# Kernel optimization log

Measured on AMD Instinct MI355X. Metric: run time of the kernel, lower is better.

Reference implementation:

```python
import jax, jax.numpy as jnp
from jax import lax
import numpy as np

INPUT_SCALE = 1.0
RES_SCALE = 1.0
RES_SIZE = 2048
INPUT_SIZE = 512
SEQ_LEN = 8192


def setup_inputs() -> dict:
    key = jax.random.key(0)
    k1, k2, k3, k4 = jax.random.split(key, 4)
    inp = jax.random.normal(k1, (SEQ_LEN, INPUT_SIZE), dtype=jnp.float32)
    state = jax.random.normal(k2, (RES_SIZE,), dtype=jnp.float32)
    W_in = jax.random.normal(k3, (RES_SIZE, INPUT_SIZE), dtype=jnp.float32)
    W_res = jax.random.normal(k4, (RES_SIZE, RES_SIZE), dtype=jnp.float32)
    return {"input": inp, "state": state, "W_in": W_in, "W_res": W_res}


def reference(input, state, W_in, W_res):
    # states[i+1] = tanh(input_scale * W_in @ input[i] + res_scale * W_res @ states[i]) / sqrt(res_size)
    inv_sqrt_n = jnp.asarray(1.0 / np.sqrt(RES_SIZE), dtype=input.dtype)
    # hoist all input projections into one GEMM: (seq_len, res_size)
    u = (INPUT_SCALE * input) @ W_in.T

    def step(s, u_t):
        s_new = jnp.tanh(u_t + RES_SCALE * (W_res @ s)) * inv_sqrt_n
        return s_new, s_new

    _, states = lax.scan(step, state, u)
    # prepend the initial state -> (seq_len+1, res_size)
    return jnp.concatenate([state[None, :], states], axis=0)
```

## Files before the change

### kernel.cpp

```cpp
#include <hip/hip_runtime.h>

#define T_SEQ   8192
#define N_RES   2048
#define K_IN    512

#define G_BLOCKS 64
#define B_THREADS 512
#define ROWS_PER_WAVE 4
#define ROWS_PER_BLOCK 32
static_assert(G_BLOCKS * ROWS_PER_BLOCK == N_RES, "row partition mismatch");

#define INV_SQRT_N 0.022097086912079612f

#define ENC_OFF 0.1f
#define ENC_THR 0.05f

typedef unsigned long long u64;
typedef unsigned int u32;
typedef float f32x2 __attribute__((ext_vector_type(2)));
typedef float f32x4 __attribute__((ext_vector_type(4)));

__device__ __forceinline__ float fast_tanh(float v) {
    float e = __expf(2.0f * v);
    return 1.0f - 2.0f / (e + 1.0f);
}

__device__ __forceinline__ void store_f4_coh(float* p, f32x4 v) {
    asm volatile("global_store_dwordx4 %0, %1, off sc0 sc1"
                 :: "v"(p), "v"(v) : "memory");
}
__device__ __forceinline__ f32x4 load_f4_coh(const float* p) {
    f32x4 r;
    asm volatile("global_load_dwordx4 %0, %1, off sc0 sc1\n\t"
                 "s_waitcnt vmcnt(0)"
                 : "=v"(r) : "v"(p) : "memory");
    return r;
}

#define KEEP2(v) asm("" : "+v"(v))

__global__ __launch_bounds__(B_THREADS, 2)
void reservoir_v11(const float* __restrict__ input,
                   const float* __restrict__ state0,
                   const float* __restrict__ W_in,
                   const float* __restrict__ W_res,
                   float* __restrict__ out,
                   float* __restrict__ ring)
{
    const int tid  = threadIdx.x;
    const int lane = tid & 63;
    const int wave = tid >> 6;
    const int blk  = blockIdx.x;
    const int r0   = blk * ROWS_PER_BLOCK + wave * ROWS_PER_WAVE;

    __shared__ float s_lds[2][N_RES];

    f32x2 wr2[ROWS_PER_WAVE][16];
    f32x2 wi2[ROWS_PER_WAVE][4];
    #pragma unroll
    for (int k = 0; k < ROWS_PER_WAVE; ++k) {
        const float* rrow = W_res + (size_t)(r0 + k) * N_RES;
        #pragma unroll
        for (int i = 0; i < 8; ++i) {
            float4 w = *reinterpret_cast<const float4*>(rrow + 4 * lane + 256 * i);
            wr2[k][2 * i]     = (f32x2){w.x, w.y};
            wr2[k][2 * i + 1] = (f32x2){w.z, w.w};
        }
        const float* irow = W_in + (size_t)(r0 + k) * K_IN;
        #pragma unroll
        for (int i = 0; i < 2; ++i) {
            float4 w = *reinterpret_cast<const float4*>(irow + 4 * lane + 256 * i);
            wi2[k][2 * i]     = (f32x2){w.x, w.y};
            wi2[k][2 * i + 1] = (f32x2){w.z, w.w};
        }
    }

    if (blk == 0)
        for (int j = tid; j < N_RES; j += B_THREADS) out[j] = state0[j];

    #pragma unroll
    for (int i = 0; i < 4; ++i)
        s_lds[0][i * 512 + tid] = state0[i * 512 + tid];

    f32x2 xv[4];
    {
        float4 a = *reinterpret_cast<const float4*>(input + 4 * lane);
        float4 b = *reinterpret_cast<const float4*>(input + 4 * lane + 256);
        xv[0] = (f32x2){a.x, a.y}; xv[1] = (f32x2){a.z, a.w};
        xv[2] = (f32x2){b.x, b.y}; xv[3] = (f32x2){b.z, b.w};
    }

    for (int t = 0; t < T_SEQ; ++t) {
        const int buf = t & 1;

        f32x2 xn[4] = {xv[0], xv[1], xv[2], xv[3]};
        if (t + 1 < T_SEQ) {
            const float* xr = input + (size_t)(t + 1) * K_IN;
            float4 a = *reinterpret_cast<const float4*>(xr + 4 * lane);
            float4 b = *reinterpret_cast<const float4*>(xr + 4 * lane + 256);
            xn[0] = (f32x2){a.x, a.y}; xn[1] = (f32x2){a.z, a.w};
            xn[2] = (f32x2){b.x, b.y}; xn[3] = (f32x2){b.z, b.w};
        }

        if (t > 0) {
            const float phi = ((t >> 1) & 1) ? -1.0f : 1.0f;
            const float* rp = ring + (buf << 11) + 4 * tid;
            f32x4 e;
            for (;;) {
                e = load_f4_coh(rp);
                if (phi * e.x > ENC_THR && phi * e.y > ENC_THR &&
                    phi * e.z > ENC_THR && phi * e.w > ENC_THR) break;
                __builtin_amdgcn_s_sleep(1);
            }
            float4 sv = make_float4(fmaf(phi, e.x, -ENC_OFF),
                                    fmaf(phi, e.y, -ENC_OFF),
                                    fmaf(phi, e.z, -ENC_OFF),
                                    fmaf(phi, e.w, -ENC_OFF));
            *reinterpret_cast<float4*>(&s_lds[buf][4 * tid]) = sv;
        }
        __syncthreads();

        f32x2 sp[16];
        #pragma unroll
        for (int i = 0; i < 8; ++i) {
            float4 s = *reinterpret_cast<const float4*>(&s_lds[buf][4 * lane + 256 * i]);
            sp[2 * i]     = (f32x2){s.x, s.y};
            sp[2 * i + 1] = (f32x2){s.z, s.w};
        }

        f32x2 acc2[ROWS_PER_WAVE];
        #pragma unroll
        for (int k = 0; k < ROWS_PER_WAVE; ++k) {
            f32x2 a = (f32x2){0.0f, 0.0f};
            #pragma unroll
            for (int i = 0; i < 4; ++i)
                a = __builtin_elementwise_fma(wi2[k][i], xv[i], a);
            #pragma unroll
            for (int i = 0; i < 16; ++i)
                a = __builtin_elementwise_fma(wr2[k][i], sp[i], a);
            acc2[k] = a;
        }

        float acc[ROWS_PER_WAVE];
        #pragma unroll
        for (int k = 0; k < ROWS_PER_WAVE; ++k) acc[k] = acc2[k].x + acc2[k].y;
        #pragma unroll
        for (int off = 32; off > 0; off >>= 1) {
            #pragma unroll
            for (int k = 0; k < ROWS_PER_WAVE; ++k)
                acc[k] += __shfl_xor(acc[k], off, 64);
        }

        const float v0 = fast_tanh(acc[0]) * INV_SQRT_N;
        const float v1 = fast_tanh(acc[1]) * INV_SQRT_N;
        const float v2 = fast_tanh(acc[2]) * INV_SQRT_N;
        const float v3 = fast_tanh(acc[3]) * INV_SQRT_N;
        const int   slotn = (t + 1) & 1;
        const float phin  = (((t + 1) >> 1) & 1) ? -1.0f : 1.0f;
        if (lane == 0) {
            f32x4 pk = {phin * (v0 + ENC_OFF), phin * (v1 + ENC_OFF),
                        phin * (v2 + ENC_OFF), phin * (v3 + ENC_OFF)};
            store_f4_coh(ring + (slotn << 11) + r0, pk);
        } else if (lane == 2) {
            *reinterpret_cast<float4*>(out + (size_t)(t + 1) * N_RES + r0) =
                make_float4(v0, v1, v2, v3);
        }

        #pragma unroll
        for (int k = 0; k < ROWS_PER_WAVE; ++k) {
            #pragma unroll
            for (int i = 0; i < 16; ++i) KEEP2(wr2[k][i]);
            #pragma unroll
            for (int i = 0; i < 4; ++i)  KEEP2(wi2[k][i]);
        }

        #pragma unroll
        for (int i = 0; i < 4; ++i) xv[i] = xn[i];
    }
}

extern "C" void kernel_launch(void* const* d_in, const int* in_sizes, int n_in,
                              void* d_out, int out_size, void* d_ws, size_t ws_size,
                              hipStream_t stream) {
    const float* input  = (const float*)d_in[0];
    const float* state0 = (const float*)d_in[1];
    const float* W_in   = (const float*)d_in[2];
    const float* W_res  = (const float*)d_in[3];
    float* out  = (float*)d_out;
    float* ring = (float*)d_ws;

    hipMemsetAsync(d_ws, 0, 2 * N_RES * sizeof(float), stream);

    void* args[] = { (void*)&input, (void*)&state0, (void*)&W_in, (void*)&W_res,
                     (void*)&out, (void*)&ring };
    hipLaunchCooperativeKernel((const void*)reservoir_v11,
                               dim3(G_BLOCKS), dim3(B_THREADS),
                               args, 0, stream);
}
```

Baseline: 16.84 ms.

## Poll ring directly per wave and fuse arrival with FMA, drop LDS barrier

Each wave now polls the full state vector from the global ring itself, in eight chunks loaded with coherent loads. It accumulates each chunk into the dot products as soon as that chunk's encoded values are valid, and re-polls only the chunks still pending. This removes the LDS staging, the block-wide __syncthreads and the serial wait on the whole vector. The shuffle reduction is also replaced with a DPP-based wave sum plus readlane. The cost is eight times more global polling traffic per block, since every wave reads all 2048 values instead of each thread reading four.

```diff
diff --git a/kernel.cpp b/kernel.cpp
--- a/kernel.cpp
+++ b/kernel.cpp
@@ -25,22 +25,34 @@
     return 1.0f - 2.0f / (e + 1.0f);
 }
 
+#define ISSUE4(dst, ptr, OFFSTR) \
+    asm volatile("global_load_dwordx4 %0, %1, off offset:" OFFSTR " sc0 sc1" \
+                 : "=v"(dst) : "v"(ptr))
+
 __device__ __forceinline__ void store_f4_coh(float* p, f32x4 v) {
     asm volatile("global_store_dwordx4 %0, %1, off sc0 sc1"
                  :: "v"(p), "v"(v) : "memory");
 }
-__device__ __forceinline__ f32x4 load_f4_coh(const float* p) {
-    f32x4 r;
-    asm volatile("global_load_dwordx4 %0, %1, off sc0 sc1\n\t"
-                 "s_waitcnt vmcnt(0)"
-                 : "=v"(r) : "v"(p) : "memory");
-    return r;
+
+template<int CTRL>
+__device__ __forceinline__ float dpp_add(float a) {
+    int s = __builtin_amdgcn_update_dpp(0, __float_as_int(a), CTRL, 0xf, 0xf, false);
+    return a + __int_as_float(s);
+}
+__device__ __forceinline__ float wave_sum(float a) {
+    a = dpp_add<0x111>(a);
+    a = dpp_add<0x112>(a);
+    a = dpp_add<0x114>(a);
+    a = dpp_add<0x118>(a);
+    a = dpp_add<0x142>(a);
+    a = dpp_add<0x143>(a);
+    return __int_as_float(__builtin_amdgcn_readlane(__float_as_int(a), 63));
 }
 
 #define KEEP2(v) asm("" : "+v"(v))
 
 __global__ __launch_bounds__(B_THREADS, 2)
-void reservoir_v11(const float* __restrict__ input,
+void reservoir_v12(const float* __restrict__ input,
                    const float* __restrict__ state0,
                    const float* __restrict__ W_in,
                    const float* __restrict__ W_res,
@@ -53,8 +65,6 @@
     const int blk  = blockIdx.x;
     const int r0   = blk * ROWS_PER_BLOCK + wave * ROWS_PER_WAVE;
 
-    __shared__ float s_lds[2][N_RES];
-
     f32x2 wr2[ROWS_PER_WAVE][16];
     f32x2 wi2[ROWS_PER_WAVE][4];
     #pragma unroll
@@ -77,10 +87,6 @@
 
     if (blk == 0)
         for (int j = tid; j < N_RES; j += B_THREADS) out[j] = state0[j];
-
-    #pragma unroll
-    for (int i = 0; i < 4; ++i)
-        s_lds[0][i * 512 + tid] = state0[i * 512 + tid];
 
     f32x2 xv[4];
     {
@@ -91,8 +97,6 @@
     }
 
     for (int t = 0; t < T_SEQ; ++t) {
-        const int buf = t & 1;
-
         f32x2 xn[4] = {xv[0], xv[1], xv[2], xv[3]};
         if (t + 1 < T_SEQ) {
             const float* xr = input + (size_t)(t + 1) * K_IN;
@@ -102,32 +106,6 @@
             xn[2] = (f32x2){b.x, b.y}; xn[3] = (f32x2){b.z, b.w};
         }
 
-        if (t > 0) {
-            const float phi = ((t >> 1) & 1) ? -1.0f : 1.0f;
-            const float* rp = ring + (buf << 11) + 4 * tid;
-            f32x4 e;
-            for (;;) {
-                e = load_f4_coh(rp);
-                if (phi * e.x > ENC_THR && phi * e.y > ENC_THR &&
-                    phi * e.z > ENC_THR && phi * e.w > ENC_THR) break;
-                __builtin_amdgcn_s_sleep(1);
-            }
-            float4 sv = make_float4(fmaf(phi, e.x, -ENC_OFF),
-                                    fmaf(phi, e.y, -ENC_OFF),
-                                    fmaf(phi, e.z, -ENC_OFF),
-                                    fmaf(phi, e.w, -ENC_OFF));
-            *reinterpret_cast<float4*>(&s_lds[buf][4 * tid]) = sv;
-        }
-        __syncthreads();
-
-        f32x2 sp[16];
-        #pragma unroll
-        for (int i = 0; i < 8; ++i) {
-            float4 s = *reinterpret_cast<const float4*>(&s_lds[buf][4 * lane + 256 * i]);
-            sp[2 * i]     = (f32x2){s.x, s.y};
-            sp[2 * i + 1] = (f32x2){s.z, s.w};
-        }
-
         f32x2 acc2[ROWS_PER_WAVE];
         #pragma unroll
         for (int k = 0; k < ROWS_PER_WAVE; ++k) {
@@ -135,26 +113,86 @@
             #pragma unroll
             for (int i = 0; i < 4; ++i)
                 a = __builtin_elementwise_fma(wi2[k][i], xv[i], a);
-            #pragma unroll
-            for (int i = 0; i < 16; ++i)
-                a = __builtin_elementwise_fma(wr2[k][i], sp[i], a);
             acc2[k] = a;
         }
 
-        float acc[ROWS_PER_WAVE];
-        #pragma unroll
-        for (int k = 0; k < ROWS_PER_WAVE; ++k) acc[k] = acc2[k].x + acc2[k].y;
-        #pragma unroll
-        for (int off = 32; off > 0; off >>= 1) {
-            #pragma unroll
-            for (int k = 0; k < ROWS_PER_WAVE; ++k)
-                acc[k] += __shfl_xor(acc[k], off, 64);
-        }
-
-        const float v0 = fast_tanh(acc[0]) * INV_SQRT_N;
-        const float v1 = fast_tanh(acc[1]) * INV_SQRT_N;
-        const float v2 = fast_tanh(acc[2]) * INV_SQRT_N;
-        const float v3 = fast_tanh(acc[3]) * INV_SQRT_N;
+        if (t == 0) {
+            #pragma unroll
+            for (int i = 0; i < 8; ++i) {
+                float4 s = *reinterpret_cast<const float4*>(state0 + 4 * lane + 256 * i);
+                f32x2 s01 = (f32x2){s.x, s.y}, s23 = (f32x2){s.z, s.w};
+                #pragma unroll
+                for (int k = 0; k < ROWS_PER_WAVE; ++k) {
+                    acc2[k] = __builtin_elementwise_fma(wr2[k][2 * i],     s01, acc2[k]);
+                    acc2[k] = __builtin_elementwise_fma(wr2[k][2 * i + 1], s23, acc2[k]);
+                }
+            }
+        } else {
+            const float phi = ((t >> 1) & 1) ? -1.0f : 1.0f;
+            const f32x2 phi2  = {phi, phi};
+            const f32x2 noff2 = {-ENC_OFF, -ENC_OFF};
+            const float* rpA = ring + ((t & 1) << 11) + 4 * lane;
+            const float* rpB = rpA + 1024;
+            f32x4 e0, e1, e2, e3, e4, e5, e6, e7;
+            u32 pend = 0xFFu;
+
+            ISSUE4(e0, rpA, "0");    ISSUE4(e1, rpA, "1024");
+            ISSUE4(e2, rpA, "2048"); ISSUE4(e3, rpA, "3072");
+            ISSUE4(e4, rpB, "0");    ISSUE4(e5, rpB, "1024");
+            ISSUE4(e6, rpB, "2048"); ISSUE4(e7, rpB, "3072");
+
+            for (;;) {
+                asm volatile("s_waitcnt vmcnt(0)"
+                             : "+v"(e0), "+v"(e1), "+v"(e2), "+v"(e3),
+                               "+v"(e4), "+v"(e5), "+v"(e6), "+v"(e7) :: "memory");
+                __builtin_amdgcn_sched_barrier(0);
+
+                #define PROC(IBIT, eN, WIDX)                                        \
+                    if (pend & (1u << IBIT)) {                                      \
+                        float m0 = fminf(phi * eN.x, phi * eN.y);                   \
+                        float m1 = fminf(phi * eN.z, phi * eN.w);                   \
+                        if (__all(fminf(m0, m1) > ENC_THR)) {                       \
+                            f32x2 s01 = __builtin_elementwise_fma(                  \
+                                phi2, (f32x2){eN.x, eN.y}, noff2);                  \
+                            f32x2 s23 = __builtin_elementwise_fma(                  \
+                                phi2, (f32x2){eN.z, eN.w}, noff2);                  \
+                            _Pragma("unroll")                                       \
+                            for (int k = 0; k < ROWS_PER_WAVE; ++k) {               \
+                                acc2[k] = __builtin_elementwise_fma(                \
+                                    wr2[k][2 * WIDX], s01, acc2[k]);                \
+                                acc2[k] = __builtin_elementwise_fma(                \
+                                    wr2[k][2 * WIDX + 1], s23, acc2[k]);            \
+                            }                                                       \
+                            pend &= ~(1u << IBIT);                                  \
+                        }                                                           \
+                    }
+                PROC(0, e0, 0) PROC(1, e1, 1) PROC(2, e2, 2) PROC(3, e3, 3)
+                PROC(4, e4, 4) PROC(5, e5, 5) PROC(6, e6, 6) PROC(7, e7, 7)
+                #undef PROC
+
+                if (!pend) break;
+                __builtin_amdgcn_s_sleep(1);
+                if (pend & 0x01u) ISSUE4(e0, rpA, "0");
+                if (pend & 0x02u) ISSUE4(e1, rpA, "1024");
+                if (pend & 0x04u) ISSUE4(e2, rpA, "2048");
+                if (pend & 0x08u) ISSUE4(e3, rpA, "3072");
+                if (pend & 0x10u) ISSUE4(e4, rpB, "0");
+                if (pend & 0x20u) ISSUE4(e5, rpB, "1024");
+                if (pend & 0x40u) ISSUE4(e6, rpB, "2048");
+                if (pend & 0x80u) ISSUE4(e7, rpB, "3072");
+            }
+        }
+
+        const float t0 = wave_sum(acc2[0].x + acc2[0].y);
+        const float t1 = wave_sum(acc2[1].x + acc2[1].y);
+        const float t2 = wave_sum(acc2[2].x + acc2[2].y);
+        const float t3 = wave_sum(acc2[3].x + acc2[3].y);
+
+        const float v0 = fast_tanh(t0) * INV_SQRT_N;
+        const float v1 = fast_tanh(t1) * INV_SQRT_N;
+        const float v2 = fast_tanh(t2) * INV_SQRT_N;
+        const float v3 = fast_tanh(t3) * INV_SQRT_N;
+
         const int   slotn = (t + 1) & 1;
         const float phin  = (((t + 1) >> 1) & 1) ? -1.0f : 1.0f;
         if (lane == 0) {
@@ -193,7 +231,7 @@
 
     void* args[] = { (void*)&input, (void*)&state0, (void*)&W_in, (void*)&W_res,
                      (void*)&out, (void*)&ring };
-    hipLaunchCooperativeKernel((const void*)reservoir_v11,
+    hipLaunchCooperativeKernel((const void*)reservoir_v12,
                                dim3(G_BLOCKS), dim3(B_THREADS),
                                args, 0, stream);
 }
```

Result: slower. 23.09 ms (+37.1%).

## Stream W_res rows from cache each step instead of holding in registers

Applied to the files above, without the earlier changes.

Drops the register-resident copy of W_res (128 floats per lane). Each timestep now reloads the rows from global memory: two rows are prefetched with inline asm loads issued before the spin-wait on the ring, and the other two rows are loaded inline during the FMA loop. The shuffle-based reductions are replaced by a DPP row-shift reduction followed by readlane. This frees VGPRs and may lower register pressure, but it adds 32 KB of L2/MALL traffic per wave per step on the serial critical path.

```diff
diff --git a/kernel.cpp b/kernel.cpp
--- a/kernel.cpp
+++ b/kernel.cpp
@@ -37,10 +37,29 @@
     return r;
 }
 
+#define ISSUE4NC(dst, ptr, OFFSTR) \
+    asm volatile("global_load_dwordx4 %0, %1, off offset:" OFFSTR \
+                 : "=v"(dst) : "v"(ptr))
+
+template<int CTRL>
+__device__ __forceinline__ float dpp_add(float a) {
+    int s = __builtin_amdgcn_update_dpp(0, __float_as_int(a), CTRL, 0xf, 0xf, false);
+    return a + __int_as_float(s);
+}
+__device__ __forceinline__ float wave_sum(float a) {
+    a = dpp_add<0x111>(a);
+    a = dpp_add<0x112>(a);
+    a = dpp_add<0x114>(a);
+    a = dpp_add<0x118>(a);
+    a = dpp_add<0x142>(a);
+    a = dpp_add<0x143>(a);
+    return __int_as_float(__builtin_amdgcn_readlane(__float_as_int(a), 63));
+}
+
 #define KEEP2(v) asm("" : "+v"(v))
 
 __global__ __launch_bounds__(B_THREADS, 2)
-void reservoir_v11(const float* __restrict__ input,
+void reservoir_v14(const float* __restrict__ input,
                    const float* __restrict__ state0,
                    const float* __restrict__ W_in,
                    const float* __restrict__ W_res,
@@ -55,17 +74,9 @@
 
     __shared__ float s_lds[2][N_RES];
 
-    f32x2 wr2[ROWS_PER_WAVE][16];
     f32x2 wi2[ROWS_PER_WAVE][4];
     #pragma unroll
     for (int k = 0; k < ROWS_PER_WAVE; ++k) {
-        const float* rrow = W_res + (size_t)(r0 + k) * N_RES;
-        #pragma unroll
-        for (int i = 0; i < 8; ++i) {
-            float4 w = *reinterpret_cast<const float4*>(rrow + 4 * lane + 256 * i);
-            wr2[k][2 * i]     = (f32x2){w.x, w.y};
-            wr2[k][2 * i + 1] = (f32x2){w.z, w.w};
-        }
         const float* irow = W_in + (size_t)(r0 + k) * K_IN;
         #pragma unroll
         for (int i = 0; i < 2; ++i) {
@@ -74,6 +85,13 @@
             wi2[k][2 * i + 1] = (f32x2){w.z, w.w};
         }
     }
+
+    const float* w0A = W_res + (size_t)(r0 + 0) * N_RES + 4 * lane;
+    const float* w0B = w0A + 1024;
+    const float* w1A = W_res + (size_t)(r0 + 1) * N_RES + 4 * lane;
+    const float* w1B = w1A + 1024;
+    const float* w2A = W_res + (size_t)(r0 + 2) * N_RES + 4 * lane;
+    const float* w3A = W_res + (size_t)(r0 + 3) * N_RES + 4 * lane;
 
     if (blk == 0)
         for (int j = tid; j < N_RES; j += B_THREADS) out[j] = state0[j];
@@ -101,6 +119,16 @@
             xn[0] = (f32x2){a.x, a.y}; xn[1] = (f32x2){a.z, a.w};
             xn[2] = (f32x2){b.x, b.y}; xn[3] = (f32x2){b.z, b.w};
         }
+
+        f32x4 p0[8], p1[8];
+        ISSUE4NC(p0[0], w0A, "0");    ISSUE4NC(p0[1], w0A, "1024");
+        ISSUE4NC(p0[2], w0A, "2048"); ISSUE4NC(p0[3], w0A, "3072");
+        ISSUE4NC(p0[4], w0B, "0");    ISSUE4NC(p0[5], w0B, "1024");
+        ISSUE4NC(p0[6], w0B, "2048"); ISSUE4NC(p0[7], w0B, "3072");
+        ISSUE4NC(p1[0], w1A, "0");    ISSUE4NC(p1[1], w1A, "1024");
+        ISSUE4NC(p1[2], w1A, "2048"); ISSUE4NC(p1[3], w1A, "3072");
+        ISSUE4NC(p1[4], w1B, "0");    ISSUE4NC(p1[5], w1B, "1024");
+        ISSUE4NC(p1[6], w1B, "2048"); ISSUE4NC(p1[7], w1B, "3072");
 
         if (t > 0) {
             const float phi = ((t >> 1) & 1) ? -1.0f : 1.0f;
@@ -120,6 +148,14 @@
         }
         __syncthreads();
 
+        asm volatile("s_waitcnt vmcnt(0)"
+                     : "+v"(p0[0]), "+v"(p0[1]), "+v"(p0[2]), "+v"(p0[3]),
+                       "+v"(p0[4]), "+v"(p0[5]), "+v"(p0[6]), "+v"(p0[7]),
+                       "+v"(p1[0]), "+v"(p1[1]), "+v"(p1[2]), "+v"(p1[3]),
+                       "+v"(p1[4]), "+v"(p1[5]), "+v"(p1[6]), "+v"(p1[7])
+                     :: "memory");
+        __builtin_amdgcn_sched_barrier(0);
+
         f32x2 sp[16];
         #pragma unroll
         for (int i = 0; i < 8; ++i) {
@@ -135,26 +171,39 @@
             #pragma unroll
             for (int i = 0; i < 4; ++i)
                 a = __builtin_elementwise_fma(wi2[k][i], xv[i], a);
-            #pragma unroll
-            for (int i = 0; i < 16; ++i)
-                a = __builtin_elementwise_fma(wr2[k][i], sp[i], a);
             acc2[k] = a;
         }
-
-        float acc[ROWS_PER_WAVE];
-        #pragma unroll
-        for (int k = 0; k < ROWS_PER_WAVE; ++k) acc[k] = acc2[k].x + acc2[k].y;
-        #pragma unroll
-        for (int off = 32; off > 0; off >>= 1) {
-            #pragma unroll
-            for (int k = 0; k < ROWS_PER_WAVE; ++k)
-                acc[k] += __shfl_xor(acc[k], off, 64);
-        }
-
-        const float v0 = fast_tanh(acc[0]) * INV_SQRT_N;
-        const float v1 = fast_tanh(acc[1]) * INV_SQRT_N;
-        const float v2 = fast_tanh(acc[2]) * INV_SQRT_N;
-        const float v3 = fast_tanh(acc[3]) * INV_SQRT_N;
+        #pragma unroll
+        for (int i = 0; i < 8; ++i) {
+            acc2[0] = __builtin_elementwise_fma((f32x2){p0[i].x, p0[i].y},
+                                                sp[2 * i], acc2[0]);
+            acc2[0] = __builtin_elementwise_fma((f32x2){p0[i].z, p0[i].w},
+                                                sp[2 * i + 1], acc2[0]);
+            acc2[1] = __builtin_elementwise_fma((f32x2){p1[i].x, p1[i].y},
+                                                sp[2 * i], acc2[1]);
+            acc2[1] = __builtin_elementwise_fma((f32x2){p1[i].z, p1[i].w},
+                                                sp[2 * i + 1], acc2[1]);
+        }
+        #pragma unroll
+        for (int i = 0; i < 8; ++i) {
+            float4 w2 = *reinterpret_cast<const float4*>(w2A + 256 * i);
+            float4 w3 = *reinterpret_cast<const float4*>(w3A + 256 * i);
+            acc2[2] = __builtin_elementwise_fma((f32x2){w2.x, w2.y}, sp[2 * i], acc2[2]);
+            acc2[2] = __builtin_elementwise_fma((f32x2){w2.z, w2.w}, sp[2 * i + 1], acc2[2]);
+            acc2[3] = __builtin_elementwise_fma((f32x2){w3.x, w3.y}, sp[2 * i], acc2[3]);
+            acc2[3] = __builtin_elementwise_fma((f32x2){w3.z, w3.w}, sp[2 * i + 1], acc2[3]);
+        }
+
+        const float t0 = wave_sum(acc2[0].x + acc2[0].y);
+        const float t1 = wave_sum(acc2[1].x + acc2[1].y);
+        const float t2 = wave_sum(acc2[2].x + acc2[2].y);
+        const float t3 = wave_sum(acc2[3].x + acc2[3].y);
+
+        const float v0 = fast_tanh(t0) * INV_SQRT_N;
+        const float v1 = fast_tanh(t1) * INV_SQRT_N;
+        const float v2 = fast_tanh(t2) * INV_SQRT_N;
+        const float v3 = fast_tanh(t3) * INV_SQRT_N;
+
         const int   slotn = (t + 1) & 1;
         const float phin  = (((t + 1) >> 1) & 1) ? -1.0f : 1.0f;
         if (lane == 0) {
@@ -169,9 +218,7 @@
         #pragma unroll
         for (int k = 0; k < ROWS_PER_WAVE; ++k) {
             #pragma unroll
-            for (int i = 0; i < 16; ++i) KEEP2(wr2[k][i]);
-            #pragma unroll
-            for (int i = 0; i < 4; ++i)  KEEP2(wi2[k][i]);
+            for (int i = 0; i < 4; ++i) KEEP2(wi2[k][i]);
         }
 
         #pragma unroll
@@ -193,7 +240,7 @@
 
     void* args[] = { (void*)&input, (void*)&state0, (void*)&W_in, (void*)&W_res,
                      (void*)&out, (void*)&ring };
-    hipLaunchCooperativeKernel((const void*)reservoir_v11,
+    hipLaunchCooperativeKernel((const void*)reservoir_v14,
                                dim3(G_BLOCKS), dim3(B_THREADS),
                                args, 0, stream);
 }
```

Result: slower. 25.51 ms (+51.5%).

## Store W_res as fp16 in LDS and use packed fp16 dot products

Applied to the files above, without the earlier changes.

Moves the block's W_res rows out of registers into LDS as packed fp16, keeps the state vector in LDS as fp16 as well, and computes the recurrent matvec with v_dot2 fp16 instructions into fp32 accumulators. The input projection is hoisted ahead of the spin-wait so it overlaps the wait for the previous step. The cross-lane shuffle reduction is replaced by DPP row operations plus readlane. The goal is to cut register pressure and per-step ALU work, at the cost of fp16 rounding error accumulating over the recurrence and more LDS reads on every step.

```diff
diff --git a/kernel.cpp b/kernel.cpp
--- a/kernel.cpp
+++ b/kernel.cpp
@@ -15,10 +15,10 @@
 #define ENC_OFF 0.1f
 #define ENC_THR 0.05f
 
-typedef unsigned long long u64;
 typedef unsigned int u32;
 typedef float f32x2 __attribute__((ext_vector_type(2)));
 typedef float f32x4 __attribute__((ext_vector_type(4)));
+typedef _Float16 h16x2 __attribute__((ext_vector_type(2)));
 
 __device__ __forceinline__ float fast_tanh(float v) {
     float e = __expf(2.0f * v);
@@ -37,10 +37,38 @@
     return r;
 }
 
+__device__ __forceinline__ float dot2(u32 w, u32 s, float acc) {
+    h16x2 wv = __builtin_bit_cast(h16x2, w);
+    h16x2 sv = __builtin_bit_cast(h16x2, s);
+#if __has_builtin(__builtin_amdgcn_fdot2)
+    return __builtin_amdgcn_fdot2(wv, sv, acc, false);
+#else
+    return fmaf((float)wv.x, (float)sv.x, fmaf((float)wv.y, (float)sv.y, acc));
+#endif
+}
+__device__ __forceinline__ u32 pkrtz(float a, float b) {
+    return __builtin_bit_cast(u32, __builtin_amdgcn_cvt_pkrtz(a, b));
+}
+
+template<int CTRL>
+__device__ __forceinline__ float dpp_add(float a) {
+    int s = __builtin_amdgcn_update_dpp(0, __float_as_int(a), CTRL, 0xf, 0xf, false);
+    return a + __int_as_float(s);
+}
+__device__ __forceinline__ float wave_sum(float a) {
+    a = dpp_add<0x111>(a);
+    a = dpp_add<0x112>(a);
+    a = dpp_add<0x114>(a);
+    a = dpp_add<0x118>(a);
+    a = dpp_add<0x142>(a);
+    a = dpp_add<0x143>(a);
+    return __int_as_float(__builtin_amdgcn_readlane(__float_as_int(a), 63));
+}
+
 #define KEEP2(v) asm("" : "+v"(v))
 
 __global__ __launch_bounds__(B_THREADS, 2)
-void reservoir_v11(const float* __restrict__ input,
+void reservoir_v15(const float* __restrict__ input,
                    const float* __restrict__ state0,
                    const float* __restrict__ W_in,
                    const float* __restrict__ W_res,
@@ -51,22 +79,22 @@
     const int lane = tid & 63;
     const int wave = tid >> 6;
     const int blk  = blockIdx.x;
-    const int r0   = blk * ROWS_PER_BLOCK + wave * ROWS_PER_WAVE;
-
-    __shared__ float s_lds[2][N_RES];
-
-    f32x2 wr2[ROWS_PER_WAVE][16];
+    const int r0   = blk * ROWS_PER_BLOCK;
+
+    __shared__ u32 wlds[ROWS_PER_BLOCK][N_RES / 2];
+    __shared__ u32 s16[2][N_RES / 2];
+
+    for (int m = tid; m < ROWS_PER_BLOCK * (N_RES / 2); m += B_THREADS) {
+        const int row = m >> 10, p = m & 1023;
+        const float2 w = *reinterpret_cast<const float2*>(
+            W_res + (size_t)(r0 + row) * N_RES + 2 * p);
+        wlds[row][p] = pkrtz(w.x, w.y);
+    }
+
     f32x2 wi2[ROWS_PER_WAVE][4];
     #pragma unroll
     for (int k = 0; k < ROWS_PER_WAVE; ++k) {
-        const float* rrow = W_res + (size_t)(r0 + k) * N_RES;
-        #pragma unroll
-        for (int i = 0; i < 8; ++i) {
-            float4 w = *reinterpret_cast<const float4*>(rrow + 4 * lane + 256 * i);
-            wr2[k][2 * i]     = (f32x2){w.x, w.y};
-            wr2[k][2 * i + 1] = (f32x2){w.z, w.w};
-        }
-        const float* irow = W_in + (size_t)(r0 + k) * K_IN;
+        const float* irow = W_in + (size_t)(r0 + wave * ROWS_PER_WAVE + k) * K_IN;
         #pragma unroll
         for (int i = 0; i < 2; ++i) {
             float4 w = *reinterpret_cast<const float4*>(irow + 4 * lane + 256 * i);
@@ -78,9 +106,11 @@
     if (blk == 0)
         for (int j = tid; j < N_RES; j += B_THREADS) out[j] = state0[j];
 
-    #pragma unroll
-    for (int i = 0; i < 4; ++i)
-        s_lds[0][i * 512 + tid] = state0[i * 512 + tid];
+    {
+        float4 s = *reinterpret_cast<const float4*>(state0 + 4 * tid);
+        s16[0][2 * tid]     = pkrtz(s.x, s.y);
+        s16[0][2 * tid + 1] = pkrtz(s.z, s.w);
+    }
 
     f32x2 xv[4];
     {
@@ -100,6 +130,16 @@
             float4 b = *reinterpret_cast<const float4*>(xr + 4 * lane + 256);
             xn[0] = (f32x2){a.x, a.y}; xn[1] = (f32x2){a.z, a.w};
             xn[2] = (f32x2){b.x, b.y}; xn[3] = (f32x2){b.z, b.w};
+        }
+
+        f32x2 accin[ROWS_PER_WAVE];
+        #pragma unroll
+        for (int k = 0; k < ROWS_PER_WAVE; ++k) {
+            f32x2 a = (f32x2){0.0f, 0.0f};
+            #pragma unroll
+            for (int i = 0; i < 4; ++i)
+                a = __builtin_elementwise_fma(wi2[k][i], xv[i], a);
+            accin[k] = a;
         }
 
         if (t > 0) {
@@ -112,66 +152,61 @@
                     phi * e.z > ENC_THR && phi * e.w > ENC_THR) break;
                 __builtin_amdgcn_s_sleep(1);
             }
-            float4 sv = make_float4(fmaf(phi, e.x, -ENC_OFF),
-                                    fmaf(phi, e.y, -ENC_OFF),
-                                    fmaf(phi, e.z, -ENC_OFF),
-                                    fmaf(phi, e.w, -ENC_OFF));
-            *reinterpret_cast<float4*>(&s_lds[buf][4 * tid]) = sv;
+            s16[buf][2 * tid]     = pkrtz(fmaf(phi, e.x, -ENC_OFF),
+                                          fmaf(phi, e.y, -ENC_OFF));
+            s16[buf][2 * tid + 1] = pkrtz(fmaf(phi, e.z, -ENC_OFF),
+                                          fmaf(phi, e.w, -ENC_OFF));
         }
         __syncthreads();
 
-        f32x2 sp[16];
-        #pragma unroll
-        for (int i = 0; i < 8; ++i) {
-            float4 s = *reinterpret_cast<const float4*>(&s_lds[buf][4 * lane + 256 * i]);
-            sp[2 * i]     = (f32x2){s.x, s.y};
-            sp[2 * i + 1] = (f32x2){s.z, s.w};
-        }
-
-        f32x2 acc2[ROWS_PER_WAVE];
+        uint4 su[4];
+        #pragma unroll
+        for (int j = 0; j < 4; ++j)
+            su[j] = *reinterpret_cast<const uint4*>(&s16[buf][16 * lane + 4 * j]);
+
+        float acc[ROWS_PER_WAVE];
         #pragma unroll
         for (int k = 0; k < ROWS_PER_WAVE; ++k) {
-            f32x2 a = (f32x2){0.0f, 0.0f};
+            const int row = wave * ROWS_PER_WAVE + k;
+            float a = accin[k].x + accin[k].y;
             #pragma unroll
-            for (int i = 0; i < 4; ++i)
-                a = __builtin_elementwise_fma(wi2[k][i], xv[i], a);
-            #pragma unroll
-            for (int i = 0; i < 16; ++i)
-                a = __builtin_elementwise_fma(wr2[k][i], sp[i], a);
-            acc2[k] = a;
-        }
-
-        float acc[ROWS_PER_WAVE];
-        #pragma unroll
-        for (int k = 0; k < ROWS_PER_WAVE; ++k) acc[k] = acc2[k].x + acc2[k].y;
-        #pragma unroll
-        for (int off = 32; off > 0; off >>= 1) {
-            #pragma unroll
-            for (int k = 0; k < ROWS_PER_WAVE; ++k)
-                acc[k] += __shfl_xor(acc[k], off, 64);
-        }
-
-        const float v0 = fast_tanh(acc[0]) * INV_SQRT_N;
-        const float v1 = fast_tanh(acc[1]) * INV_SQRT_N;
-        const float v2 = fast_tanh(acc[2]) * INV_SQRT_N;
-        const float v3 = fast_tanh(acc[3]) * INV_SQRT_N;
+            for (int j = 0; j < 4; ++j) {
+                uint4 wu = *reinterpret_cast<const uint4*>(
+                    &wlds[row][16 * lane + 4 * j]);
+                a = dot2(wu.x, su[j].x, a);
+                a = dot2(wu.y, su[j].y, a);
+                a = dot2(wu.z, su[j].z, a);
+                a = dot2(wu.w, su[j].w, a);
+            }
+            acc[k] = a;
+        }
+
+        const float t0 = wave_sum(acc[0]);
+        const float t1 = wave_sum(acc[1]);
+        const float t2 = wave_sum(acc[2]);
+        const float t3 = wave_sum(acc[3]);
+
+        const float v0 = fast_tanh(t0) * INV_SQRT_N;
+        const float v1 = fast_tanh(t1) * INV_SQRT_N;
+        const float v2 = fast_tanh(t2) * INV_SQRT_N;
+        const float v3 = fast_tanh(t3) * INV_SQRT_N;
+
+        const int   wr0   = r0 + wave * ROWS_PER_WAVE;
         const int   slotn = (t + 1) & 1;
         const float phin  = (((t + 1) >> 1) & 1) ? -1.0f : 1.0f;
         if (lane == 0) {
             f32x4 pk = {phin * (v0 + ENC_OFF), phin * (v1 + ENC_OFF),
                         phin * (v2 + ENC_OFF), phin * (v3 + ENC_OFF)};
-            store_f4_coh(ring + (slotn << 11) + r0, pk);
+            store_f4_coh(ring + (slotn << 11) + wr0, pk);
         } else if (lane == 2) {
-            *reinterpret_cast<float4*>(out + (size_t)(t + 1) * N_RES + r0) =
+            *reinterpret_cast<float4*>(out + (size_t)(t + 1) * N_RES + wr0) =
                 make_float4(v0, v1, v2, v3);
         }
 
         #pragma unroll
         for (int k = 0; k < ROWS_PER_WAVE; ++k) {
             #pragma unroll
-            for (int i = 0; i < 16; ++i) KEEP2(wr2[k][i]);
-            #pragma unroll
-            for (int i = 0; i < 4; ++i)  KEEP2(wi2[k][i]);
+            for (int i = 0; i < 4; ++i) KEEP2(wi2[k][i]);
         }
 
         #pragma unroll
@@ -193,7 +228,7 @@
 
     void* args[] = { (void*)&input, (void*)&state0, (void*)&W_in, (void*)&W_res,
                      (void*)&out, (void*)&ring };
-    hipLaunchCooperativeKernel((const void*)reservoir_v11,
+    hipLaunchCooperativeKernel((const void*)reservoir_v15,
                                dim3(G_BLOCKS), dim3(B_THREADS),
                                args, 0, stream);
 }
```

Measured after the change: 21.71 ms. 1.29x slower.
